# Kernel optimization log

Hardware: AMD Instinct MI355X
Metric: run time of the kernel (lower is better)

The kernel has to match this reference:

```python
import jax, jax.numpy as jnp
import numpy as np

NY, NU, NH = 8, 8, 256
T, NB = 2048, 64


def setup_inputs() -> dict:
    key = jax.random.key(0)
    ks = jax.random.split(key, 10)
    return {
        "_y0": jax.random.normal(ks[0], (NB, NY), dtype=jnp.float32),
        "_U": jax.random.normal(ks[1], (T, NB, NU), dtype=jnp.float32),
        "lmbd_cont_real": jax.random.uniform(ks[2], (NH // 2,), dtype=jnp.float32),
        "lmbd_cont_imag": jax.random.uniform(ks[3], (NH // 2,), dtype=jnp.float32),
        "B": jax.random.normal(ks[4], (NH, NU), dtype=jnp.float32) / np.sqrt(NU).astype(np.float32),
        "multiplier_on_B": jnp.zeros((NH,), dtype=jnp.float32),
        "W_y2x": jax.random.normal(ks[5], (NH, NY), dtype=jnp.float32) / np.sqrt(NY).astype(np.float32),
        "b_y2x": jax.random.normal(ks[6], (NH,), dtype=jnp.float32) * 0.01,
        "W_x2y": jax.random.normal(ks[7], (NY, NH), dtype=jnp.float32) / np.sqrt(NH).astype(np.float32),
        "b_x2y": jax.random.normal(ks[8], (NY,), dtype=jnp.float32) * 0.01,
    }


def reference(_y0, _U, lmbd_cont_real, lmbd_cont_imag, B, multiplier_on_B,
              W_y2x, b_y2x, W_x2y, b_x2y):
    H2 = lmbd_cont_real.shape[0]
    # input drive: (T, NB, NH)
    Bu = jnp.einsum('tbu,hu->tbh', _U, B) * jnp.exp(multiplier_on_B)
    # stable complex-conjugate-pair eigenvalues
    r = jnp.exp(-jnp.abs(lmbd_cont_real))
    theta = (jnp.pi / 2) * lmbd_cont_imag
    re = r * jnp.cos(theta)
    im = r * jnp.sin(theta)
    # initial state from y0
    x0 = _y0 @ W_y2x.T + b_y2x  # (NB, NH)

    def step(x, bu):
        x1, x2 = x[:, :H2], x[:, H2:]
        # A = [[diag(re), -diag(im)], [diag(im), diag(re)]]; x <- x A^T + bu
        nx = jnp.concatenate([re * x1 - im * x2, im * x1 + re * x2], axis=1) + bu
        return nx, nx

    _, X = jax.lax.scan(step, x0, Bu)  # X: (T, NB, NH)
    Y = X @ W_x2y.T + b_x2y  # (T, NB, NY)
    return Y
```

## Files before the change

### kernel.cpp

```cpp
#include <hip/hip_runtime.h>
#include <math.h>

#define T_   2048
#define NB_  64
#define NU_  8
#define NY_  8
#define NH_  256
#define H2_  128
#define CCH  64
#define LCH  32

static const float PI_HALF = 1.5707963267948966f;

typedef _Float16 half8  __attribute__((ext_vector_type(8)));
typedef __fp16   fp16x2 __attribute__((ext_vector_type(2)));
typedef float    f32x4  __attribute__((ext_vector_type(4)));


__global__ __launch_bounds__(64) void k_scanproj(
    const float* __restrict__ U, const float* __restrict__ lr,
    const float* __restrict__ li, const float* __restrict__ B,
    const float* __restrict__ mult, const float* __restrict__ Wx2y,
    const float* __restrict__ bx2y, float* __restrict__ c_buf,
    float* __restrict__ Y)
{
    const int k = blockIdx.x >> 6;
    const int b = blockIdx.x & 63;
    const int j = threadIdx.x;
    const int c0 = 2*j;

    float2 lrv = *(const float2*)(lr + c0);
    float2 liv = *(const float2*)(li + c0);
    float rA  = expf(-fabsf(lrv.x)), thA = PI_HALF*liv.x;
    float reA = rA*cosf(thA), imA = rA*sinf(thA);
    float rB  = expf(-fabsf(lrv.y)), thB = PI_HALF*liv.y;
    float reB = rB*cosf(thB), imB = rB*sinf(thB);

    float Ba1[NU_], Ba2[NU_], Bb1[NU_], Bb2[NU_];
    {
        float s1 = expf(mult[c0]),     s2 = expf(mult[c0+128]);
        float s3 = expf(mult[c0+1]),   s4 = expf(mult[c0+129]);
        #pragma unroll
        for (int i = 0; i < NU_; i++) {
            Ba1[i] = B[(c0    )*NU_ + i] * s1;
            Bb1[i] = B[(c0+  1)*NU_ + i] * s3;
            Ba2[i] = B[(c0+128)*NU_ + i] * s2;
            Bb2[i] = B[(c0+129)*NU_ + i] * s4;
        }
    }

    const int yv  = j & 15;
    const int kg  = j >> 4;
    half8 wf[8];
    #pragma unroll
    for (int q = 0; q < 8; q++) {
        half8 f;
        if (yv < 8) {
            const float* wr = Wx2y + yv*NH_ + q*32 + kg*8;
            #pragma unroll
            for (int i = 0; i < 8; i++) f[i] = (_Float16)wr[i];
        } else {
            #pragma unroll
            for (int i = 0; i < 8; i++) f[i] = (_Float16)0.f;
        }
        wf[q] = f;
    }
    const float bias = bx2y[yv & 7];

    __shared__ _Float16 xS[16*256];
    uint32_t* xS32 = (uint32_t*)xS;

    float xa1=0.f, xa2=0.f, xb1=0.f, xb2=0.f;
    const float4* Ut = (const float4*)(U + ((size_t)(k*LCH)*NB_ + b)*NU_);

    float4 u0 = Ut[0], u1 = Ut[1];

    for (int s = 0; s < LCH/16; s++) {
        #pragma unroll 4
        for (int t16 = 0; t16 < 16; t16++) {
            const int t = s*16 + t16;
            float4 cu0 = u0, cu1 = u1;
            const int tn = (t < LCH-1) ? t+1 : t;
            u0 = Ut[tn*128 + 0];
            u1 = Ut[tn*128 + 1];

            float u[NU_] = {cu0.x,cu0.y,cu0.z,cu0.w,cu1.x,cu1.y,cu1.z,cu1.w};
            float ba1=0.f, ba2=0.f, bb1=0.f, bb2=0.f;
            #pragma unroll
            for (int i = 0; i < NU_; i++) {
                ba1 = fmaf(u[i], Ba1[i], ba1);
                ba2 = fmaf(u[i], Ba2[i], ba2);
                bb1 = fmaf(u[i], Bb1[i], bb1);
                bb2 = fmaf(u[i], Bb2[i], bb2);
            }
            float na1 = fmaf(reA, xa1, fmaf(-imA, xa2, ba1));
            float na2 = fmaf(imA, xa1, fmaf( reA, xa2, ba2));
            float nb1 = fmaf(reB, xb1, fmaf(-imB, xb2, bb1));
            float nb2 = fmaf(imB, xb1, fmaf( reB, xb2, bb2));
            xa1=na1; xa2=na2; xb1=nb1; xb2=nb2;

            union { fp16x2 h; uint32_t u32; } p0, p1;
            p0.h = __builtin_amdgcn_cvt_pkrtz(xa1, xb1);
            p1.h = __builtin_amdgcn_cvt_pkrtz(xa2, xb2);
            const int w0 = t16*128 + (((j>>2) ^ t16) << 2) + (j & 3);
            xS32[w0]      = p0.u32;
            xS32[w0 + 64] = p1.u32;
        }
        __syncthreads();

        f32x4 acc = {0.f, 0.f, 0.f, 0.f};
        #pragma unroll
        for (int q = 0; q < 8; q++) {
            const int p = ((q << 2) + kg) ^ yv;
            const half8* ap = (const half8*)(xS + (yv << 8) + (p << 3));
            acc = __builtin_amdgcn_mfma_f32_16x16x32_f16(*ap, wf[q], acc, 0, 0, 0);
        }
        __syncthreads();

        if (yv < 8) {
            #pragma unroll
            for (int r = 0; r < 4; r++) {
                const int tg = k*LCH + s*16 + kg*4 + r;
                Y[((size_t)tg*NB_ + b)*NY_ + yv] = acc[r] + bias;
            }
        }
    }

    *(float4*)(c_buf + ((size_t)(k*NB_ + b))*(H2_*2) + 4*j) =
        make_float4(xa1, xa2, xb1, xb2);
}

__global__ __launch_bounds__(64) void k_prefix(
    const float* __restrict__ y0, const float* __restrict__ lr,
    const float* __restrict__ li, const float* __restrict__ Wy2x,
    const float* __restrict__ by2x, const float* __restrict__ c_buf,
    uint32_t* __restrict__ initT)
{
    const int g = blockIdx.x*64 + threadIdx.x;
    const int b = g >> 7;
    const int h = g & 127;

    float x1 = by2x[h], x2 = by2x[h+H2_];
    #pragma unroll
    for (int y = 0; y < NY_; y++) {
        float yy = y0[b*NY_ + y];
        x1 = fmaf(yy, Wy2x[h*NY_ + y],        x1);
        x2 = fmaf(yy, Wy2x[(h+H2_)*NY_ + y],  x2);
    }

    float rL  = expf(-(float)LCH * fabsf(lr[h]));
    float thL = (float)LCH * PI_HALF * li[h];
    float reL = rL * cosf(thL), imL = rL * sinf(thL);

    #pragma unroll 8
    for (int k = 0; k < CCH; k++) {
        float2 c = *(const float2*)(c_buf + (size_t)k*16384 + b*256 + 2*h);
        union { fp16x2 hh; uint32_t u32; } pk;
        pk.hh = __builtin_amdgcn_cvt_pkrtz(x1, x2);
        initT[(size_t)k*8192 + b*128 + h] = pk.u32;
        float n1 = fmaf(reL, x1, fmaf(-imL, x2, c.x));
        float n2 = fmaf(imL, x1, fmaf( reL, x2, c.y));
        x1 = n1; x2 = n2;
    }
}

__global__ __launch_bounds__(64) void k_mcoef(
    const float* __restrict__ lr, const float* __restrict__ li,
    const float* __restrict__ Wx2y, uint32_t* __restrict__ M32)
{
    const int R = blockIdx.x;
    const int dlt = R >> 3, y = R & 7;
    const float e = (float)(dlt + 1);
    const int j = threadIdx.x;

    #pragma unroll
    for (int hh = 0; hh < 2; hh++) {
        const int h = j + hh*64;
        float r  = expf(-e * fabsf(lr[h]));
        float an = e * PI_HALF * li[h];
        float c = r * cosf(an), s = r * sinf(an);
        float W1 = Wx2y[y*NH_ + h];
        float W2 = Wx2y[y*NH_ + h + H2_];
        float Mre = fmaf(W1, c,  W2 * s);
        float Mim = fmaf(W2, c, -W1 * s);
        union { fp16x2 hh2; uint32_t u32; } pk;
        pk.hh2 = __builtin_amdgcn_cvt_pkrtz(Mre, Mim);
        M32[R*128 + hh*64 + j] = pk.u32;
    }
}

__global__ __launch_bounds__(256) void k_corr(
    const _Float16* __restrict__ M, const uint32_t* __restrict__ initT,
    float* __restrict__ Y)
{
    const int k    = blockIdx.x >> 1;
    const int half = blockIdx.x & 1;
    const int tid  = threadIdx.x;
    const int w    = tid >> 6, l = tid & 63;
    const int lane16 = l & 15, kg = l >> 4;

    __shared__ _Float16 bS[32*264];
    {
        uint32_t* bS32 = (uint32_t*)bS;
        const int r = tid >> 3, seg = tid & 7;
        const uint32_t* src = initT + (size_t)k*8192 + (half*32 + r)*128 + seg*16;
        uint32_t* dst = bS32 + r*132 + seg*16;
        ((uint4*)dst)[0] = ((const uint4*)src)[0];
        ((uint4*)dst)[1] = ((const uint4*)src)[1];
        ((uint4*)dst)[2] = ((const uint4*)src)[2];
        ((uint4*)dst)[3] = ((const uint4*)src)[3];
    }
    __syncthreads();

    #pragma unroll
    for (int rt = 0; rt < 4; rt++) {
        const int R0 = w*64 + rt*16;
        half8 af[8];
        #pragma unroll
        for (int q = 0; q < 8; q++)
            af[q] = *(const half8*)(M + (size_t)(R0 + lane16)*256 + q*32 + kg*8);

        f32x4 acc0 = {0.f,0.f,0.f,0.f}, acc1 = {0.f,0.f,0.f,0.f};
        #pragma unroll
        for (int q = 0; q < 8; q++) {
            const half8* b0 = (const half8*)(bS + ( 0 + lane16)*264 + q*32 + kg*8);
            const half8* b1 = (const half8*)(bS + (16 + lane16)*264 + q*32 + kg*8);
            acc0 = __builtin_amdgcn_mfma_f32_16x16x32_f16(af[q], *b0, acc0, 0, 0, 0);
            acc1 = __builtin_amdgcn_mfma_f32_16x16x32_f16(af[q], *b1, acc1, 0, 0, 0);
        }

        #pragma unroll
        for (int r4 = 0; r4 < 4; r4++) {
            const int R = R0 + kg*4 + r4;
            const int t = k*LCH + (R >> 3);
            const int y = R & 7;
            float* yp0 = Y + ((size_t)t*NB_ + half*32 +  0 + lane16)*NY_ + y;
            float* yp1 = Y + ((size_t)t*NB_ + half*32 + 16 + lane16)*NY_ + y;
            *yp0 += acc0[r4];
            *yp1 += acc1[r4];
        }
    }
}

extern "C" void kernel_launch(void* const* d_in, const int* in_sizes, int n_in,
                              void* d_out, int out_size, void* d_ws, size_t ws_size,
                              hipStream_t stream) {
    const float* y0   = (const float*)d_in[0];
    const float* U    = (const float*)d_in[1];
    const float* lr   = (const float*)d_in[2];
    const float* li   = (const float*)d_in[3];
    const float* B    = (const float*)d_in[4];
    const float* mult = (const float*)d_in[5];
    const float* Wy2x = (const float*)d_in[6];
    const float* by2x = (const float*)d_in[7];
    const float* Wx2y = (const float*)d_in[8];
    const float* bx2y = (const float*)d_in[9];
    float* Y = (float*)d_out;

    uint32_t*  Mbuf  = (uint32_t*)d_ws;
    float*     c_buf = (float*)((char*)d_ws + (128<<10));
    uint32_t*  initT = (uint32_t*)((char*)d_ws + (128<<10) + (4<<20));

    k_mcoef   <<<256, 64, 0, stream>>>(lr, li, Wx2y, Mbuf);
    k_scanproj<<<CCH*NB_, 64, 0, stream>>>(U, lr, li, B, mult, Wx2y, bx2y, c_buf, Y);
    k_prefix  <<<(NB_*H2_)/64, 64, 0, stream>>>(y0, lr, li, Wy2x, by2x, c_buf, initT);
    k_corr    <<<CCH*2, 256, 0, stream>>>((const _Float16*)Mbuf, initT, Y);
}
```

Baseline: 108.1 us.

## Widen scan blocks to 128 threads, stage U in LDS, merge prefix and mcoef kernels

The chunked scan kernel now uses 128 threads per block, one per complex channel instead of two. U for the chunk is staged once in shared memory, and the output projection is split across two waves with a reduction through shared memory. The prefix and M-coefficient kernels are merged into one launch to save a kernel launch. The correction kernel's Y updates are vectorised to float4 read-modify-writes. The aim is more parallelism per chunk and less launch overhead, at the cost of extra syncs and LDS traffic.

```diff
diff --git a/kernel.cpp b/kernel.cpp
--- a/kernel.cpp
+++ b/kernel.cpp
@@ -17,175 +17,177 @@
 typedef float    f32x4  __attribute__((ext_vector_type(4)));
 
 
-__global__ __launch_bounds__(64) void k_scanproj(
+__global__ __launch_bounds__(128) void k_scanproj(
     const float* __restrict__ U, const float* __restrict__ lr,
     const float* __restrict__ li, const float* __restrict__ B,
     const float* __restrict__ mult, const float* __restrict__ Wx2y,
     const float* __restrict__ bx2y, float* __restrict__ c_buf,
     float* __restrict__ Y)
 {
-    const int k = blockIdx.x >> 6;
-    const int b = blockIdx.x & 63;
-    const int j = threadIdx.x;
-    const int c0 = 2*j;
-
-    float2 lrv = *(const float2*)(lr + c0);
-    float2 liv = *(const float2*)(li + c0);
-    float rA  = expf(-fabsf(lrv.x)), thA = PI_HALF*liv.x;
-    float reA = rA*cosf(thA), imA = rA*sinf(thA);
-    float rB  = expf(-fabsf(lrv.y)), thB = PI_HALF*liv.y;
-    float reB = rB*cosf(thB), imB = rB*sinf(thB);
-
-    float Ba1[NU_], Ba2[NU_], Bb1[NU_], Bb2[NU_];
+    const int k   = blockIdx.x >> 6;
+    const int b   = blockIdx.x & 63;
+    const int tid = threadIdx.x;
+    const int h   = tid;
+    const int w   = tid >> 6;
+    const int l   = tid & 63;
+    const int row = l & 15;
+    const int kg  = (l >> 4) & 3;
+
+    float rr = expf(-fabsf(lr[h]));
+    float th = PI_HALF * li[h];
+    float re = rr * cosf(th), im = rr * sinf(th);
+
+    float B1[NU_], B2[NU_];
     {
-        float s1 = expf(mult[c0]),     s2 = expf(mult[c0+128]);
-        float s3 = expf(mult[c0+1]),   s4 = expf(mult[c0+129]);
-        #pragma unroll
-        for (int i = 0; i < NU_; i++) {
-            Ba1[i] = B[(c0    )*NU_ + i] * s1;
-            Bb1[i] = B[(c0+  1)*NU_ + i] * s3;
-            Ba2[i] = B[(c0+128)*NU_ + i] * s2;
-            Bb2[i] = B[(c0+129)*NU_ + i] * s4;
-        }
-    }
-
-    const int yv  = j & 15;
-    const int kg  = j >> 4;
-    half8 wf[8];
+        float s1 = expf(mult[h]), s2 = expf(mult[h+H2_]);
+        float4 b1a = *(const float4*)(B + h*NU_);
+        float4 b1b = *(const float4*)(B + h*NU_ + 4);
+        float4 b2a = *(const float4*)(B + (h+H2_)*NU_);
+        float4 b2b = *(const float4*)(B + (h+H2_)*NU_ + 4);
+        B1[0]=b1a.x*s1; B1[1]=b1a.y*s1; B1[2]=b1a.z*s1; B1[3]=b1a.w*s1;
+        B1[4]=b1b.x*s1; B1[5]=b1b.y*s1; B1[6]=b1b.z*s1; B1[7]=b1b.w*s1;
+        B2[0]=b2a.x*s2; B2[1]=b2a.y*s2; B2[2]=b2a.z*s2; B2[3]=b2a.w*s2;
+        B2[4]=b2b.x*s2; B2[5]=b2b.y*s2; B2[6]=b2b.z*s2; B2[7]=b2b.w*s2;
+    }
+
+    half8 wf[4];
     #pragma unroll
-    for (int q = 0; q < 8; q++) {
-        half8 f;
-        if (yv < 8) {
-            const float* wr = Wx2y + yv*NH_ + q*32 + kg*8;
+    for (int q2 = 0; q2 < 4; q2++) {
+        const int q = 4*w + q2;
+        union { uint32_t u32[4]; half8 h8; } fu;
+        if (row < 8) {
+            const int hh = q*16 + kg*4;
+            const float* lo = Wx2y + row*NH_ + hh;
+            const float* hi = lo + H2_;
             #pragma unroll
-            for (int i = 0; i < 8; i++) f[i] = (_Float16)wr[i];
+            for (int i = 0; i < 4; i++) {
+                union { fp16x2 h2; uint32_t u; } pk;
+                pk.h2 = __builtin_amdgcn_cvt_pkrtz(lo[i], hi[i]);
+                fu.u32[i] = pk.u;
+            }
         } else {
-            #pragma unroll
-            for (int i = 0; i < 8; i++) f[i] = (_Float16)0.f;
-        }
-        wf[q] = f;
-    }
-    const float bias = bx2y[yv & 7];
-
+            fu.u32[0]=0; fu.u32[1]=0; fu.u32[2]=0; fu.u32[3]=0;
+        }
+        wf[q2] = fu.h8;
+    }
+    const float bias = bx2y[tid & 7];
+
+    __shared__ float    uS[LCH*NU_];
     __shared__ _Float16 xS[16*256];
+    __shared__ float    pS[4*132];
     uint32_t* xS32 = (uint32_t*)xS;
 
-    float xa1=0.f, xa2=0.f, xb1=0.f, xb2=0.f;
-    const float4* Ut = (const float4*)(U + ((size_t)(k*LCH)*NB_ + b)*NU_);
-
-    float4 u0 = Ut[0], u1 = Ut[1];
-
-    for (int s = 0; s < LCH/16; s++) {
+    if (tid < 64) {
+        ((float4*)uS)[tid] =
+            *(const float4*)(U + ((size_t)(k*LCH + (tid>>1))*NB_ + b)*NU_ + (tid&1)*4);
+    }
+    __syncthreads();
+
+    float x1 = 0.f, x2 = 0.f;
+    const int g = h >> 2;
+
+    for (int s = 0; s < 2; s++) {
         #pragma unroll 4
         for (int t16 = 0; t16 < 16; t16++) {
             const int t = s*16 + t16;
-            float4 cu0 = u0, cu1 = u1;
-            const int tn = (t < LCH-1) ? t+1 : t;
-            u0 = Ut[tn*128 + 0];
-            u1 = Ut[tn*128 + 1];
-
-            float u[NU_] = {cu0.x,cu0.y,cu0.z,cu0.w,cu1.x,cu1.y,cu1.z,cu1.w};
-            float ba1=0.f, ba2=0.f, bb1=0.f, bb2=0.f;
+            float4 u0 = ((const float4*)uS)[2*t+0];
+            float4 u1 = ((const float4*)uS)[2*t+1];
+            float u[NU_] = {u0.x,u0.y,u0.z,u0.w,u1.x,u1.y,u1.z,u1.w};
+            float bu1=0.f, bu2=0.f;
             #pragma unroll
             for (int i = 0; i < NU_; i++) {
-                ba1 = fmaf(u[i], Ba1[i], ba1);
-                ba2 = fmaf(u[i], Ba2[i], ba2);
-                bb1 = fmaf(u[i], Bb1[i], bb1);
-                bb2 = fmaf(u[i], Bb2[i], bb2);
+                bu1 = fmaf(u[i], B1[i], bu1);
+                bu2 = fmaf(u[i], B2[i], bu2);
             }
-            float na1 = fmaf(reA, xa1, fmaf(-imA, xa2, ba1));
-            float na2 = fmaf(imA, xa1, fmaf( reA, xa2, ba2));
-            float nb1 = fmaf(reB, xb1, fmaf(-imB, xb2, bb1));
-            float nb2 = fmaf(imB, xb1, fmaf( reB, xb2, bb2));
-            xa1=na1; xa2=na2; xb1=nb1; xb2=nb2;
-
-            union { fp16x2 h; uint32_t u32; } p0, p1;
-            p0.h = __builtin_amdgcn_cvt_pkrtz(xa1, xb1);
-            p1.h = __builtin_amdgcn_cvt_pkrtz(xa2, xb2);
-            const int w0 = t16*128 + (((j>>2) ^ t16) << 2) + (j & 3);
-            xS32[w0]      = p0.u32;
-            xS32[w0 + 64] = p1.u32;
+            float n1 = fmaf(re, x1, fmaf(-im, x2, bu1));
+            float n2 = fmaf(im, x1, fmaf( re, x2, bu2));
+            x1 = n1; x2 = n2;
+
+            union { fp16x2 h2; uint32_t u32; } pk;
+            pk.h2 = __builtin_amdgcn_cvt_pkrtz(x1, x2);
+            xS32[t16*128 + ((g ^ t16) & 31)*4 + (h & 3)] = pk.u32;
         }
         __syncthreads();
 
-        f32x4 acc = {0.f, 0.f, 0.f, 0.f};
-        #pragma unroll
-        for (int q = 0; q < 8; q++) {
-            const int p = ((q << 2) + kg) ^ yv;
-            const half8* ap = (const half8*)(xS + (yv << 8) + (p << 3));
-            acc = __builtin_amdgcn_mfma_f32_16x16x32_f16(*ap, wf[q], acc, 0, 0, 0);
-        }
+        f32x4 acc = {0.f,0.f,0.f,0.f};
+        #pragma unroll
+        for (int q2 = 0; q2 < 4; q2++) {
+            const int q = 4*w + q2;
+            const int p = ((q << 2) + kg) ^ row;
+            const half8* ap = (const half8*)(xS + (row << 8) + (p << 3));
+            acc = __builtin_amdgcn_mfma_f32_16x16x32_f16(*ap, wf[q2], acc, 0, 0, 0);
+        }
+        #pragma unroll
+        for (int r = 0; r < 4; r++) pS[r*132 + w*64 + l] = acc[r];
         __syncthreads();
 
-        if (yv < 8) {
-            #pragma unroll
-            for (int r = 0; r < 4; r++) {
-                const int tg = k*LCH + s*16 + kg*4 + r;
-                Y[((size_t)tg*NB_ + b)*NY_ + yv] = acc[r] + bias;
-            }
-        }
-    }
-
-    *(float4*)(c_buf + ((size_t)(k*NB_ + b))*(H2_*2) + 4*j) =
-        make_float4(xa1, xa2, xb1, xb2);
-}
-
-__global__ __launch_bounds__(64) void k_prefix(
+        {
+            const int t  = tid >> 3, y = tid & 7;
+            const int ls = ((t >> 2) << 4) + y;
+            const int rg = t & 3;
+            float sum = pS[rg*132 + ls] + pS[rg*132 + 64 + ls];
+            Y[((size_t)(k*LCH + s*16 + t)*NB_ + b)*NY_ + y] = sum + bias;
+        }
+    }
+
+    *(float2*)(c_buf + (size_t)(k*NB_ + b)*(H2_*2) + 2*h) = make_float2(x1, x2);
+}
+
+__global__ __launch_bounds__(64) void k_mid(
     const float* __restrict__ y0, const float* __restrict__ lr,
     const float* __restrict__ li, const float* __restrict__ Wy2x,
-    const float* __restrict__ by2x, const float* __restrict__ c_buf,
-    uint32_t* __restrict__ initT)
+    const float* __restrict__ by2x, const float* __restrict__ Wx2y,
+    const float* __restrict__ c_buf, uint32_t* __restrict__ initT,
+    uint32_t* __restrict__ M32)
 {
-    const int g = blockIdx.x*64 + threadIdx.x;
-    const int b = g >> 7;
-    const int h = g & 127;
-
-    float x1 = by2x[h], x2 = by2x[h+H2_];
-    #pragma unroll
-    for (int y = 0; y < NY_; y++) {
-        float yy = y0[b*NY_ + y];
-        x1 = fmaf(yy, Wy2x[h*NY_ + y],        x1);
-        x2 = fmaf(yy, Wy2x[(h+H2_)*NY_ + y],  x2);
-    }
-
-    float rL  = expf(-(float)LCH * fabsf(lr[h]));
-    float thL = (float)LCH * PI_HALF * li[h];
-    float reL = rL * cosf(thL), imL = rL * sinf(thL);
-
-    #pragma unroll 8
-    for (int k = 0; k < CCH; k++) {
-        float2 c = *(const float2*)(c_buf + (size_t)k*16384 + b*256 + 2*h);
-        union { fp16x2 hh; uint32_t u32; } pk;
-        pk.hh = __builtin_amdgcn_cvt_pkrtz(x1, x2);
-        initT[(size_t)k*8192 + b*128 + h] = pk.u32;
-        float n1 = fmaf(reL, x1, fmaf(-imL, x2, c.x));
-        float n2 = fmaf(imL, x1, fmaf( reL, x2, c.y));
-        x1 = n1; x2 = n2;
-    }
-}
-
-__global__ __launch_bounds__(64) void k_mcoef(
-    const float* __restrict__ lr, const float* __restrict__ li,
-    const float* __restrict__ Wx2y, uint32_t* __restrict__ M32)
-{
-    const int R = blockIdx.x;
-    const int dlt = R >> 3, y = R & 7;
-    const float e = (float)(dlt + 1);
-    const int j = threadIdx.x;
-
-    #pragma unroll
-    for (int hh = 0; hh < 2; hh++) {
-        const int h = j + hh*64;
-        float r  = expf(-e * fabsf(lr[h]));
-        float an = e * PI_HALF * li[h];
-        float c = r * cosf(an), s = r * sinf(an);
-        float W1 = Wx2y[y*NH_ + h];
-        float W2 = Wx2y[y*NH_ + h + H2_];
-        float Mre = fmaf(W1, c,  W2 * s);
-        float Mim = fmaf(W2, c, -W1 * s);
-        union { fp16x2 hh2; uint32_t u32; } pk;
-        pk.hh2 = __builtin_amdgcn_cvt_pkrtz(Mre, Mim);
-        M32[R*128 + hh*64 + j] = pk.u32;
+    const int bi = blockIdx.x;
+    const int j  = threadIdx.x;
+
+    if (bi < 128) {
+        const int gidx = bi*64 + j;
+        const int b = gidx >> 7;
+        const int h = gidx & 127;
+
+        float x1 = by2x[h], x2 = by2x[h+H2_];
+        #pragma unroll
+        for (int y = 0; y < NY_; y++) {
+            float yy = y0[b*NY_ + y];
+            x1 = fmaf(yy, Wy2x[h*NY_ + y],        x1);
+            x2 = fmaf(yy, Wy2x[(h+H2_)*NY_ + y],  x2);
+        }
+
+        float rL  = expf(-(float)LCH * fabsf(lr[h]));
+        float thL = (float)LCH * PI_HALF * li[h];
+        float reL = rL * cosf(thL), imL = rL * sinf(thL);
+
+        #pragma unroll 8
+        for (int k = 0; k < CCH; k++) {
+            float2 c = *(const float2*)(c_buf + (size_t)k*16384 + b*256 + 2*h);
+            union { fp16x2 hh; uint32_t u32; } pk;
+            pk.hh = __builtin_amdgcn_cvt_pkrtz(x1, x2);
+            initT[(size_t)k*8192 + b*128 + h] = pk.u32;
+            float n1 = fmaf(reL, x1, fmaf(-imL, x2, c.x));
+            float n2 = fmaf(imL, x1, fmaf( reL, x2, c.y));
+            x1 = n1; x2 = n2;
+        }
+    } else {
+        const int R = bi - 128;
+        const int dlt = R >> 3, y = R & 7;
+        const float e = (float)(dlt + 1);
+        #pragma unroll
+        for (int hh = 0; hh < 2; hh++) {
+            const int h = j + hh*64;
+            float r  = expf(-e * fabsf(lr[h]));
+            float an = e * PI_HALF * li[h];
+            float c = r * cosf(an), sn = r * sinf(an);
+            float W1 = Wx2y[y*NH_ + h];
+            float W2 = Wx2y[y*NH_ + h + H2_];
+            float Mre = fmaf(W1, c,  W2 * sn);
+            float Mim = fmaf(W2, c, -W1 * sn);
+            union { fp16x2 h2; uint32_t u32; } pk;
+            pk.h2 = __builtin_amdgcn_cvt_pkrtz(Mre, Mim);
+            M32[R*128 + hh*64 + j] = pk.u32;
+        }
     }
 }
 
@@ -229,16 +231,14 @@
             acc1 = __builtin_amdgcn_mfma_f32_16x16x32_f16(af[q], *b1, acc1, 0, 0, 0);
         }
 
-        #pragma unroll
-        for (int r4 = 0; r4 < 4; r4++) {
-            const int R = R0 + kg*4 + r4;
-            const int t = k*LCH + (R >> 3);
-            const int y = R & 7;
-            float* yp0 = Y + ((size_t)t*NB_ + half*32 +  0 + lane16)*NY_ + y;
-            float* yp1 = Y + ((size_t)t*NB_ + half*32 + 16 + lane16)*NY_ + y;
-            *yp0 += acc0[r4];
-            *yp1 += acc1[r4];
-        }
+        const int t  = k*LCH + (R0 >> 3) + (kg >> 1);
+        const int y0 = (kg & 1) * 4;
+        float4* yp0 = (float4*)(Y + ((size_t)t*NB_ + half*32 +  0 + lane16)*NY_ + y0);
+        float4* yp1 = (float4*)(Y + ((size_t)t*NB_ + half*32 + 16 + lane16)*NY_ + y0);
+        float4 o0 = *yp0, o1 = *yp1;
+        o0.x += acc0[0]; o0.y += acc0[1]; o0.z += acc0[2]; o0.w += acc0[3];
+        o1.x += acc1[0]; o1.y += acc1[1]; o1.z += acc1[2]; o1.w += acc1[3];
+        *yp0 = o0; *yp1 = o1;
     }
 }
 
@@ -257,12 +257,11 @@
     const float* bx2y = (const float*)d_in[9];
     float* Y = (float*)d_out;
 
-    uint32_t*  Mbuf  = (uint32_t*)d_ws;
-    float*     c_buf = (float*)((char*)d_ws + (128<<10));
-    uint32_t*  initT = (uint32_t*)((char*)d_ws + (128<<10) + (4<<20));
-
-    k_mcoef   <<<256, 64, 0, stream>>>(lr, li, Wx2y, Mbuf);
-    k_scanproj<<<CCH*NB_, 64, 0, stream>>>(U, lr, li, B, mult, Wx2y, bx2y, c_buf, Y);
-    k_prefix  <<<(NB_*H2_)/64, 64, 0, stream>>>(y0, lr, li, Wy2x, by2x, c_buf, initT);
+    uint32_t* Mbuf  = (uint32_t*)d_ws;
+    float*    c_buf = (float*)((char*)d_ws + (128<<10));
+    uint32_t* initT = (uint32_t*)((char*)d_ws + (128<<10) + (4<<20));
+
+    k_scanproj<<<CCH*NB_, 128, 0, stream>>>(U, lr, li, B, mult, Wx2y, bx2y, c_buf, Y);
+    k_mid     <<<384, 64, 0, stream>>>(y0, lr, li, Wy2x, by2x, Wx2y, c_buf, initT, Mbuf);
     k_corr    <<<CCH*2, 256, 0, stream>>>((const _Float16*)Mbuf, initT, Y);
 }
```

After: 104.5 us. 1.03x faster.
